# Optimization experiments

Hardware: AMD Instinct MI355X
Metric: run time of the kernel (lower is better)

Reference implementation:

```python
import jax, jax.numpy as jnp
import numpy as np

MARGIN = 0.2
EPS = 1e-6  # F.pairwise_distance default eps (added to the difference)


def _cdist(x):
    # Euclidean pairwise distances, [N, N]
    sq = jnp.sum(x * x, axis=1)
    d2 = sq[:, None] + sq[None, :] - 2.0 * (x @ x.T)
    return jnp.sqrt(jnp.maximum(d2, 0.0))


def setup_inputs() -> dict:
    key = jax.random.key(0)
    k1, k2 = jax.random.split(key)
    features = jax.random.normal(k1, (8192, 128), dtype=jnp.float32)
    labels = jax.random.randint(k2, (8192,), 0, 512)
    return {"features": features, "labels": labels}


def reference(features, labels):
    # Distances are used only for (non-differentiable) index selection.
    dists = jax.lax.stop_gradient(_cdist(features))
    pos_mask = labels[None, :] == labels[:, None]  # includes diagonal (self), as in the torch loop
    neg_mask = ~pos_mask

    # Batch-hard mining, vectorized over all anchor rows:
    # hardest positive = max dist among same-label; hardest negative = min dist among different-label.
    pos_idx = jnp.argmax(jnp.where(pos_mask, dists, -jnp.inf), axis=1)
    neg_idx = jnp.argmin(jnp.where(neg_mask, dists, jnp.inf), axis=1)
    # Anchor is skipped in the original loop only if it has no negatives.
    valid = jnp.any(neg_mask, axis=1)

    anchors = features
    pos = features[pos_idx]
    neg = features[neg_idx]

    # F.pairwise_distance(x1, x2, p=2) == ||x1 - x2 + eps||_2
    pos_d = jnp.linalg.norm(anchors - pos + EPS, axis=1)
    neg_d = jnp.linalg.norm(anchors - neg + EPS, axis=1)
    per_anchor = jax.nn.relu(pos_d - neg_d + MARGIN)

    cnt = jnp.sum(valid)
    loss = jnp.where(
        cnt > 0,
        jnp.sum(jnp.where(valid, per_anchor, 0.0)) / jnp.maximum(cnt, 1).astype(per_anchor.dtype),
        jnp.zeros((), per_anchor.dtype),
    )
    return loss
```

## Files before the change

### kernel.cpp

```cpp
#include <hip/hip_runtime.h>
#include <hip/hip_bf16.h>

#define N 8192
#define DIMS 128
#define NSLICE 32
#define SLICE_COLS (N / NSLICE)
#define SUBTILES (SLICE_COLS / 16)
#define NSTEPS (SUBTILES / 2)
#define ROWS_PER_BLOCK 128
#define STRIPS 2
#define NROWBLK (N / ROWS_PER_BLOCK)
#define NFIN 2048
#define MARGIN_F 0.2f
#define EPS_F 1e-6f
#define BIAS_F 512.0f
#define META_LDS 16384
#define INF_F __builtin_huge_valf()

typedef __bf16 bf16x8 __attribute__((ext_vector_type(8)));
typedef float f32x4 __attribute__((ext_vector_type(4)));

#define XB_OFF   0
#define META_OFF 2097152
#define PART_OFF 2162688
#define BSUM_OFF 4259840

#define GLD_LDS(g, l) \
  __builtin_amdgcn_global_load_lds( \
      (const __attribute__((address_space(1))) void*)(g), \
      (__attribute__((address_space(3))) void*)(l), 16, 0, 0)

__global__ __launch_bounds__(256) void prep_kernel(
    const float* __restrict__ feat, const int* __restrict__ lab,
    unsigned short* __restrict__ Xb, float2* __restrict__ meta) {
  int row = blockIdx.x * 4 + (threadIdx.x >> 6);
  int lane = threadIdx.x & 63;
  float2 x = *reinterpret_cast<const float2*>(feat + (size_t)row * DIMS + lane * 2);
  __hip_bfloat16 hx = __float2bfloat16(x.x);
  __hip_bfloat16 hy = __float2bfloat16(x.y);
  unsigned short ux, uy;
  __builtin_memcpy(&ux, &hx, 2);
  __builtin_memcpy(&uy, &hy, 2);
  unsigned int packed = (unsigned int)ux | ((unsigned int)uy << 16);
  *reinterpret_cast<unsigned int*>(Xb + (size_t)row * DIMS + lane * 2) = packed;
  float s = x.x * x.x + x.y * x.y;
#pragma unroll
  for (int m = 32; m >= 1; m >>= 1) s += __shfl_xor(s, m, 64);
  if (lane == 0) meta[row] = make_float2(s + BIAS_F, __int_as_float(lab[row]));
}

__global__ __launch_bounds__(256, 4) void mine_kernel(
    const unsigned short* __restrict__ Xb, const float2* __restrict__ meta,
    const int* __restrict__ lab, uint2* __restrict__ part) {
  __shared__ char smem[2 * 8192 + 2048];

  int rb = blockIdx.x / NSLICE;
  int sl = blockIdx.x % NSLICE;
  int tid = threadIdx.x;
  int wave = tid >> 6;
  int lane = tid & 63;
  int lrow = lane & 15;
  int lk = lane >> 4;
  int rowbase = rb * ROWS_PER_BLOCK + wave * (STRIPS * 16);
  int j0 = sl * SLICE_COLS;

  if (wave < 2) {
    const char* g = (const char*)meta + (size_t)j0 * 8 + tid * 16;
    char* l = smem + META_LDS + wave * 1024;
    GLD_LDS(g, l);
  }
  int colt = tid >> 4;
  int chunk = tid & 15;
  const char* gsrc0 = (const char*)Xb + (size_t)(j0 + colt) * 256 +
                      ((chunk ^ (colt & 7)) * 16);
  {
    GLD_LDS(gsrc0, smem + wave * 1024);
    GLD_LDS(gsrc0 + 4096, smem + 4096 + wave * 1024);
  }

  bf16x8 afrag[STRIPS][4];
#pragma unroll
  for (int s = 0; s < STRIPS; ++s) {
    const unsigned short* rp = Xb + (size_t)(rowbase + s * 16 + lrow) * DIMS;
#pragma unroll
    for (int g = 0; g < 4; ++g)
      afrag[s][g] = *reinterpret_cast<const bf16x8*>(rp + g * 32 + lk * 8);
  }
  int4 labi[STRIPS];
#pragma unroll
  for (int s = 0; s < STRIPS; ++s)
    labi[s] = *reinterpret_cast<const int4*>(lab + rowbase + s * 16 + lk * 4);

  unsigned int bpu[STRIPS][4], bnu[STRIPS][4];
#pragma unroll
  for (int s = 0; s < STRIPS; ++s)
#pragma unroll
    for (int e = 0; e < 4; ++e) { bpu[s][e] = 0u; bnu[s][e] = 0xFFFFFFFFu; }

  int boff[4];
#pragma unroll
  for (int g = 0; g < 4; ++g)
    boff[g] = lrow * 256 + (((g * 4 + lk) ^ (lrow & 7)) * 16);

  __syncthreads();

  for (int it = 0; it < NSTEPS; ++it) {
    int cur = it & 1;
    if (it + 1 < NSTEPS) {
      const char* g = gsrc0 + (size_t)(it + 1) * 8192;
      char* l = smem + (cur ^ 1) * 8192 + wave * 1024;
      GLD_LDS(g, l);
      GLD_LDS(g + 4096, l + 4096);
    }

#pragma unroll
    for (int h = 0; h < 2; ++h) {
      int t = it * 2 + h;
      float2 mcur =
          *reinterpret_cast<const float2*>(smem + META_LDS + t * 128 + lrow * 8);
      float sqjB = mcur.x;
      int labj = __float_as_int(mcur.y);
      unsigned int ju = (unsigned int)(j0 + t * 16 + lrow);

      const char* bbase = smem + cur * 8192 + h * 4096;
      bf16x8 bb[4];
#pragma unroll
      for (int g = 0; g < 4; ++g)
        bb[g] = *reinterpret_cast<const bf16x8*>(bbase + boff[g]);

#pragma unroll
      for (int s = 0; s < STRIPS; ++s) {
        f32x4 acc = {0.f, 0.f, 0.f, 0.f};
#pragma unroll
        for (int g = 0; g < 4; ++g)
          acc = __builtin_amdgcn_mfma_f32_16x16x32_bf16(afrag[s][g], bb[g], acc,
                                                        0, 0, 0);
        int labs[4] = {labi[s].x, labi[s].y, labi[s].z, labi[s].w};
#pragma unroll
        for (int e = 0; e < 4; ++e) {
          float key = fmaf(-2.0f, acc[e], sqjB);
          unsigned int u = (__float_as_uint(key) & 0xFFFFE000u) | ju;
          bool pos = (labj == labs[e]);
          unsigned int up = pos ? u : 0u;
          unsigned int un = pos ? 0xFFFFFFFFu : u;
          bpu[s][e] = max(bpu[s][e], up);
          bnu[s][e] = min(bnu[s][e], un);
        }
      }
    }
    __syncthreads();
  }

#pragma unroll
  for (int s = 0; s < STRIPS; ++s) {
#pragma unroll
    for (int e = 0; e < 4; ++e) {
      unsigned int pu = bpu[s][e], nu = bnu[s][e];
#pragma unroll
      for (int m = 1; m < 16; m <<= 1) {
        pu = max(pu, (unsigned int)__shfl_xor((int)pu, m, 64));
        nu = min(nu, (unsigned int)__shfl_xor((int)nu, m, 64));
      }
      if (lrow == 0) {
        int row = rowbase + s * 16 + lk * 4 + e;
        part[(size_t)sl * N + row] = make_uint2(pu, nu);
      }
    }
  }
}

__global__ __launch_bounds__(256) void finalize_kernel(
    const float* __restrict__ feat, const uint2* __restrict__ part,
    float2* __restrict__ bsum) {
  int wave = threadIdx.x >> 6, lane = threadIdx.x & 63;
  int i = blockIdx.x * 4 + wave;

  unsigned int pu = 0u, nu = 0xFFFFFFFFu;
  if (lane < NSLICE) {
    uint2 p = part[(size_t)lane * N + i];
    pu = p.x; nu = p.y;
  }
#pragma unroll
  for (int m = 1; m < NSLICE; m <<= 1) {
    pu = max(pu, (unsigned int)__shfl_xor((int)pu, m, 64));
    nu = min(nu, (unsigned int)__shfl_xor((int)nu, m, 64));
  }
  pu = (unsigned int)__shfl((int)pu, 0, 64);
  nu = (unsigned int)__shfl((int)nu, 0, 64);
  bool valid = (nu != 0xFFFFFFFFu);
  int pi = (int)(pu & 8191u);
  int ni = (int)(nu & 8191u);

  float2 av = *reinterpret_cast<const float2*>(feat + (size_t)i * DIMS + lane * 2);
  float2 pw = *reinterpret_cast<const float2*>(feat + (size_t)pi * DIMS + lane * 2);
  float2 nw = *reinterpret_cast<const float2*>(feat + (size_t)ni * DIMS + lane * 2);
  float d0 = av.x - pw.x + EPS_F, d1 = av.y - pw.y + EPS_F;
  float sp = fmaf(d0, d0, d1 * d1);
  float e0 = av.x - nw.x + EPS_F, e1 = av.y - nw.y + EPS_F;
  float sn = fmaf(e0, e0, e1 * e1);
#pragma unroll
  for (int m = 32; m >= 1; m >>= 1) {
    sp += __shfl_xor(sp, m, 64);
    sn += __shfl_xor(sn, m, 64);
  }

  __shared__ float s_s[4], s_c[4];
  if (lane == 0) {
    float per = sqrtf(sp) - sqrtf(sn) + MARGIN_F;
    per = per > 0.f ? per : 0.f;
    per = valid ? per : 0.f;
    s_s[wave] = per;
    s_c[wave] = valid ? 1.f : 0.f;
  }
  __syncthreads();
  if (threadIdx.x == 0) {
    float ts = (s_s[0] + s_s[1]) + (s_s[2] + s_s[3]);
    float tc = (s_c[0] + s_c[1]) + (s_c[2] + s_c[3]);
    bsum[blockIdx.x] = make_float2(ts, tc);
  }
}

__global__ __launch_bounds__(256) void final_reduce_kernel(
    const float2* __restrict__ bsum, float* __restrict__ out) {
  int t = threadIdx.x;
  float s = 0.f, c = 0.f;
#pragma unroll
  for (int k = 0; k < NFIN / 256; ++k) {
    float2 v = bsum[t + k * 256];
    s += v.x; c += v.y;
  }
#pragma unroll
  for (int m = 32; m >= 1; m >>= 1) {
    s += __shfl_xor(s, m, 64);
    c += __shfl_xor(c, m, 64);
  }
  __shared__ float s_s[4], s_c[4];
  int wave = t >> 6, lane = t & 63;
  if (lane == 0) { s_s[wave] = s; s_c[wave] = c; }
  __syncthreads();
  if (t == 0) {
    float ts = (s_s[0] + s_s[1]) + (s_s[2] + s_s[3]);
    float tc = (s_c[0] + s_c[1]) + (s_c[2] + s_c[3]);
    out[0] = (tc > 0.f) ? (ts / tc) : 0.f;
  }
}

extern "C" void kernel_launch(void* const* d_in, const int* in_sizes, int n_in,
                              void* d_out, int out_size, void* d_ws, size_t ws_size,
                              hipStream_t stream) {
  const float* feat = (const float*)d_in[0];
  const int* lab = (const int*)d_in[1];
  char* ws = (char*)d_ws;
  unsigned short* Xb = (unsigned short*)(ws + XB_OFF);
  float2* meta = (float2*)(ws + META_OFF);
  uint2* part = (uint2*)(ws + PART_OFF);
  float2* bsum = (float2*)(ws + BSUM_OFF);
  float* out = (float*)d_out;

  prep_kernel<<<N / 4, 256, 0, stream>>>(feat, lab, Xb, meta);
  mine_kernel<<<NROWBLK * NSLICE, 256, 0, stream>>>(Xb, meta, lab, part);
  finalize_kernel<<<N / 4, 256, 0, stream>>>(feat, part, bsum);
  final_reduce_kernel<<<1, 256, 0, stream>>>(bsum, out);
}
```

Baseline: 46.26 us.

## Split mining columns into 64 slices and break MFMA accumulation dependency

Doubles the number of column slices in the mining kernel, so there are twice as many blocks, each scanning half as many columns. This shrinks the metadata staging and widens the finalize reduction to all 64 lanes. The B-fragment and meta LDS reads for both half-steps are hoisted ahead of the MFMAs, and each dot product is split into two independent accumulator chains, to shorten the dependent MFMA latency. In exchange, the partial-result buffer doubles in size, and each block runs a shorter pipelined loop over which to amortise its A-fragment loads.

```diff
diff --git a/kernel.cpp b/kernel.cpp
--- a/kernel.cpp
+++ b/kernel.cpp
@@ -3,7 +3,7 @@
 
 #define N 8192
 #define DIMS 128
-#define NSLICE 32
+#define NSLICE 64
 #define SLICE_COLS (N / NSLICE)
 #define SUBTILES (SLICE_COLS / 16)
 #define NSTEPS (SUBTILES / 2)
@@ -23,7 +23,7 @@
 #define XB_OFF   0
 #define META_OFF 2097152
 #define PART_OFF 2162688
-#define BSUM_OFF 4259840
+#define BSUM_OFF 6553600
 
 #define GLD_LDS(g, l) \
   __builtin_amdgcn_global_load_lds( \
@@ -52,7 +52,7 @@
 __global__ __launch_bounds__(256, 4) void mine_kernel(
     const unsigned short* __restrict__ Xb, const float2* __restrict__ meta,
     const int* __restrict__ lab, uint2* __restrict__ part) {
-  __shared__ char smem[2 * 8192 + 2048];
+  __shared__ char smem[2 * 8192 + 1024];
 
   int rb = blockIdx.x / NSLICE;
   int sl = blockIdx.x % NSLICE;
@@ -64,9 +64,9 @@
   int rowbase = rb * ROWS_PER_BLOCK + wave * (STRIPS * 16);
   int j0 = sl * SLICE_COLS;
 
-  if (wave < 2) {
+  if (tid < 64) {
     const char* g = (const char*)meta + (size_t)j0 * 8 + tid * 16;
-    char* l = smem + META_LDS + wave * 1024;
+    char* l = smem + META_LDS;
     GLD_LDS(g, l);
   }
   int colt = tid >> 4;
@@ -113,28 +113,35 @@
       GLD_LDS(g + 4096, l + 4096);
     }
 
+    int t0 = it * 2, t1 = it * 2 + 1;
+    float2 m0 = *reinterpret_cast<const float2*>(smem + META_LDS + t0 * 128 + lrow * 8);
+    float2 m1 = *reinterpret_cast<const float2*>(smem + META_LDS + t1 * 128 + lrow * 8);
+    const char* bbase = smem + cur * 8192;
+    bf16x8 b0[4], b1[4];
+#pragma unroll
+    for (int g = 0; g < 4; ++g) {
+      b0[g] = *reinterpret_cast<const bf16x8*>(bbase + boff[g]);
+      b1[g] = *reinterpret_cast<const bf16x8*>(bbase + 4096 + boff[g]);
+    }
+
 #pragma unroll
     for (int h = 0; h < 2; ++h) {
-      int t = it * 2 + h;
-      float2 mcur =
-          *reinterpret_cast<const float2*>(smem + META_LDS + t * 128 + lrow * 8);
-      float sqjB = mcur.x;
-      int labj = __float_as_int(mcur.y);
+      const bf16x8* bb = h ? b1 : b0;
+      float2 mc = h ? m1 : m0;
+      int t = h ? t1 : t0;
+      float sqjB = mc.x;
+      int labj = __float_as_int(mc.y);
       unsigned int ju = (unsigned int)(j0 + t * 16 + lrow);
 
-      const char* bbase = smem + cur * 8192 + h * 4096;
-      bf16x8 bb[4];
-#pragma unroll
-      for (int g = 0; g < 4; ++g)
-        bb[g] = *reinterpret_cast<const bf16x8*>(bbase + boff[g]);
-
 #pragma unroll
       for (int s = 0; s < STRIPS; ++s) {
-        f32x4 acc = {0.f, 0.f, 0.f, 0.f};
-#pragma unroll
-        for (int g = 0; g < 4; ++g)
-          acc = __builtin_amdgcn_mfma_f32_16x16x32_bf16(afrag[s][g], bb[g], acc,
-                                                        0, 0, 0);
+        f32x4 za = {0.f, 0.f, 0.f, 0.f};
+        f32x4 zb = {0.f, 0.f, 0.f, 0.f};
+        za = __builtin_amdgcn_mfma_f32_16x16x32_bf16(afrag[s][0], bb[0], za, 0, 0, 0);
+        zb = __builtin_amdgcn_mfma_f32_16x16x32_bf16(afrag[s][1], bb[1], zb, 0, 0, 0);
+        za = __builtin_amdgcn_mfma_f32_16x16x32_bf16(afrag[s][2], bb[2], za, 0, 0, 0);
+        zb = __builtin_amdgcn_mfma_f32_16x16x32_bf16(afrag[s][3], bb[3], zb, 0, 0, 0);
+        f32x4 acc = za + zb;
         int labs[4] = {labi[s].x, labi[s].y, labi[s].z, labi[s].w};
 #pragma unroll
         for (int e = 0; e < 4; ++e) {
@@ -175,13 +182,10 @@
   int wave = threadIdx.x >> 6, lane = threadIdx.x & 63;
   int i = blockIdx.x * 4 + wave;
 
-  unsigned int pu = 0u, nu = 0xFFFFFFFFu;
-  if (lane < NSLICE) {
-    uint2 p = part[(size_t)lane * N + i];
-    pu = p.x; nu = p.y;
-  }
-#pragma unroll
-  for (int m = 1; m < NSLICE; m <<= 1) {
+  uint2 p = part[(size_t)lane * N + i];
+  unsigned int pu = p.x, nu = p.y;
+#pragma unroll
+  for (int m = 1; m < 64; m <<= 1) {
     pu = max(pu, (unsigned int)__shfl_xor((int)pu, m, 64));
     nu = min(nu, (unsigned int)__shfl_xor((int)nu, m, 64));
   }
```

Result: slower. 55.04 us (+19.0%).
